# Kernel tuning notes

Hardware: AMD Instinct MI355X
Metric: run time of the kernel (lower is better)

The kernel has to match this reference:

```python
import jax, jax.numpy as jnp
import numpy as np
import math

B, S, D, H = 2, 2048, 1024, 16
HD = D // H  # 64


def setup_inputs() -> dict:
    key = jax.random.key(0)
    ks = jax.random.split(key, 12)
    s = 1.0 / math.sqrt(D)
    inp = {
        "x": jax.random.normal(ks[0], (B, S, D), dtype=jnp.float32),
        "Wq": jax.random.normal(ks[1], (D, D), dtype=jnp.float32) * s,
        "bq": jnp.zeros((D,), dtype=jnp.float32),
        "Wk": jax.random.normal(ks[2], (D, D), dtype=jnp.float32) * s,
        "bk": jnp.zeros((D,), dtype=jnp.float32),
        "Wv": jax.random.normal(ks[3], (D, D), dtype=jnp.float32) * s,
        "bv": jnp.zeros((D,), dtype=jnp.float32),
        "Wo": jax.random.normal(ks[4], (D, D), dtype=jnp.float32) * s,
        "bo": jnp.zeros((D,), dtype=jnp.float32),
        "cross_modal_weights": jnp.ones((3, 3), dtype=jnp.float32),
        "mask": jax.random.randint(ks[5], (B, S, S), 0, 2, dtype=jnp.int32),
        "modality_info": jax.random.randint(ks[6], (B, S), 0, 3, dtype=jnp.int64),
    }
    return inp


def reference(x, Wq, bq, Wk, bk, Wv, bv, Wo, bo, cross_modal_weights, mask, modality_info):
    b, s, d = x.shape
    # QKV projections -> [b, H, s, HD]
    q = (x @ Wq + bq).reshape(b, s, H, HD).transpose(0, 2, 1, 3)
    k = (x @ Wk + bk).reshape(b, s, H, HD).transpose(0, 2, 1, 3)
    v = (x @ Wv + bv).reshape(b, s, H, HD).transpose(0, 2, 1, 3)
    scores = jnp.einsum("bhqd,bhkd->bhqk", q, k) / math.sqrt(HD)
    # modality bias: torch uses .item() -> detached scalar
    modality_bias = jax.lax.stop_gradient(jnp.mean(cross_modal_weights))
    scores = scores + modality_bias
    # user mask [b, s, s] broadcast over heads; masked_fill(mask==0, -1e9)
    scores = jnp.where(mask[:, None, :, :] == 0, jnp.float32(-1e9), scores)
    attn = jax.nn.softmax(scores, axis=-1)
    # dropout_rate = 0.0 (eval) -> identity
    ctx = jnp.einsum("bhqk,bhkd->bhqd", attn, v)
    ctx = ctx.transpose(0, 2, 1, 3).reshape(b, s, d)
    return ctx @ Wo + bo
```

## Files before the change

kernel.cpp:

```cpp
#include <hip/hip_runtime.h>
#include <math.h>

#define Bdim 2
#define Sdim 2048
#define Ddim 1024
#define Hnum 16
#define HDdim 64
#define Kdim 1024

using short8   = __attribute__((ext_vector_type(8))) short;
using ushort8  = __attribute__((ext_vector_type(8))) unsigned short;
using ushort4v = __attribute__((ext_vector_type(4))) unsigned short;
using floatx4  = __attribute__((ext_vector_type(4))) float;
using half4    = __attribute__((ext_vector_type(4))) _Float16;
using half2v   = __attribute__((ext_vector_type(2))) _Float16;

__device__ __forceinline__ unsigned short f2bf(float f) {
    __bf16 b = (__bf16)f;
    return __builtin_bit_cast(unsigned short, b);
}

__device__ __forceinline__ void async_ld16(const unsigned short* g, unsigned short* l) {
    __builtin_amdgcn_global_load_lds(
        (const __attribute__((address_space(1))) unsigned int*)(g),
        (__attribute__((address_space(3))) unsigned int*)(l), 16, 0, 0);
}

__global__ __launch_bounds__(256) void prep_kernel(
    const float* __restrict__ x,
    const float* __restrict__ Wq, const float* __restrict__ Wk,
    const float* __restrict__ Wv, const float* __restrict__ Wo,
    const int* __restrict__ mask,
    unsigned short* __restrict__ xb, unsigned short* __restrict__ Wt,
    unsigned long long* __restrict__ packed)
{
    __shared__ float tile[64][65];
    const int bid = blockIdx.x;
    const int t   = threadIdx.x;

    if (bid < 2048) {
        size_t i = ((size_t)bid * 256 + t) * 8;
        float4 a = *(const float4*)(x + i);
        float4 b = *(const float4*)(x + i + 4);
        ushort8 o;
        o[0] = f2bf(a.x); o[1] = f2bf(a.y); o[2] = f2bf(a.z); o[3] = f2bf(a.w);
        o[4] = f2bf(b.x); o[5] = f2bf(b.y); o[6] = f2bf(b.z); o[7] = f2bf(b.w);
        *(ushort8*)(xb + i) = o;
    } else if (bid < 3072) {
        const int idx = bid - 2048;
        const int n0 = (idx & 15) * 64;
        const int k0 = ((idx >> 4) & 15) * 64;
        const int z  = idx >> 8;
        const float* W = (z == 0) ? Wq : (z == 1) ? Wk : (z == 2) ? Wv : Wo;
        unsigned short* outp = Wt + (size_t)z * Kdim * Ddim;
#pragma unroll
        for (int i = 0; i < 4; ++i) {
            int flat = i * 256 + t;
            int r = flat >> 4;
            int c = (flat & 15) * 4;
            float4 v = *(const float4*)(W + (size_t)(k0 + r) * Ddim + n0 + c);
            tile[r][c] = v.x; tile[r][c+1] = v.y; tile[r][c+2] = v.z; tile[r][c+3] = v.w;
        }
        __syncthreads();
#pragma unroll
        for (int i = 0; i < 16; ++i) {
            int flat = i * 256 + t;
            int n = flat >> 6;
            int k = flat & 63;
            outp[(size_t)(n0 + n) * Kdim + k0 + k] = f2bf(tile[k][n]);
        }
    } else {
        const int lane = t & 63;
        const int l15  = lane & 15;
        const int quad = lane >> 4;
        const unsigned int gid = (bid - 3072) * 4 + (t >> 6);
        const int b  = gid >> 14;
        const int qg = (gid >> 7) & 127;
        const int kb = gid & 127;
        int4 mv = *(const int4*)(mask + ((size_t)(b * Sdim) + qg * 16 + l15) * Sdim + kb * 16 + quad * 4);
        unsigned long long w0 = __ballot(mv.x != 0);
        unsigned long long w1 = __ballot(mv.y != 0);
        unsigned long long w2 = __ballot(mv.z != 0);
        unsigned long long w3 = __ballot(mv.w != 0);
        if (lane == 0) {
            unsigned long long* dst = packed + (size_t)gid * 4;
            dst[0] = w0; dst[1] = w1; dst[2] = w2; dst[3] = w3;
        }
    }
}

#define MFMA_NORM(MT, NT) acc[MT][NT] = __builtin_amdgcn_mfma_f32_16x16x32_bf16(af[MT], bfr[NT], acc[MT][NT], 0, 0, 0)
#define MFMA_SWAP(MT, NT) acc[MT][NT] = __builtin_amdgcn_mfma_f32_16x16x32_bf16(bfr[NT], af[MT], acc[MT][NT], 0, 0, 0)

#define GEMM_KLOOP(APTR, WPTR, NT_TILES, MFMA_STMT)                              \
    for (int kt = 0; kt < 16; ++kt) {                                            \
        const int k0 = kt * 64;                                                  \
        __syncthreads();                                                         \
        _Pragma("unroll")                                                        \
        for (int i = 0; i < 4; ++i) {                                            \
            int flat = i * 256 + t;                                              \
            int row  = flat >> 3;                                                \
            int cg   = (flat & 7) ^ (row & 7);                                   \
            async_ld16(APTR + (size_t)(m0 + row) * Kdim + k0 + cg * 8,           \
                       As + flat * 8);                                           \
        }                                                                        \
        _Pragma("unroll")                                                        \
        for (int i = 0; i < NT_TILES; ++i) {                                     \
            int flat = i * 256 + t;                                              \
            int row  = flat >> 3;                                                \
            int cg   = (flat & 7) ^ (row & 7);                                   \
            async_ld16(WPTR + (size_t)row * Kdim + k0 + cg * 8,                  \
                       Bs + flat * 8);                                           \
        }                                                                        \
        __syncthreads();                                                         \
        _Pragma("unroll")                                                        \
        for (int ks = 0; ks < 2; ++ks) {                                         \
            short8 af[4], bfr[NT_TILES];                                         \
            _Pragma("unroll")                                                    \
            for (int mt = 0; mt < 4; ++mt) {                                     \
                int row = wm * 64 + mt * 16 + l15;                               \
                int ch  = (ks * 4 + quad) ^ (row & 7);                           \
                af[mt] = *(const short8*)(As + row * 64 + ch * 8);               \
            }                                                                    \
            _Pragma("unroll")                                                    \
            for (int nt = 0; nt < NT_TILES; ++nt) {                              \
                int row = wn * (NT_TILES * 16) + nt * 16 + l15;                  \
                int ch  = (ks * 4 + quad) ^ (row & 7);                           \
                bfr[nt] = *(const short8*)(Bs + row * 64 + ch * 8);              \
            }                                                                    \
            _Pragma("unroll")                                                    \
            for (int mt = 0; mt < 4; ++mt)                                       \
                _Pragma("unroll")                                                \
                for (int nt = 0; nt < NT_TILES; ++nt)                            \
                    MFMA_STMT(mt, nt);                                           \
        }                                                                        \
    }

__global__ __launch_bounds__(256, 4) void qkv_mfma_kernel(
    const unsigned short* __restrict__ A, const unsigned short* __restrict__ Wt,
    const float* __restrict__ bq, const float* __restrict__ bk, const float* __restrict__ bv,
    unsigned short* __restrict__ qo, unsigned short* __restrict__ ko, _Float16* __restrict__ vto)
{
    __shared__ __align__(16) unsigned short As[128 * 64];
    __shared__ __align__(16) unsigned short Bs[128 * 64];
    const int lin = blockIdx.y * 24 + blockIdx.x;
    const int xcd = lin & 7;
    const int idx = lin >> 3;
    const int bx  = (xcd & 1) * 12 + idx % 12;
    const int by  = (xcd >> 1) * 8 + idx / 12;
    const int n0   = bx * 128;
    const int m0   = by * 128;
    const int wsel = n0 >> 10;
    const int c0   = n0 & 1023;
    const unsigned short* Wp = Wt + (size_t)wsel * Kdim * Ddim + (size_t)c0 * Kdim;

    const int t    = threadIdx.x;
    const int lane = t & 63;
    const int w    = t >> 6;
    const int quad = lane >> 4;
    const int l15  = lane & 15;
    const int wm   = w & 1;
    const int wn   = w >> 1;
    floatx4 acc[4][4];
#pragma unroll
    for (int mt = 0; mt < 4; ++mt)
#pragma unroll
        for (int nt = 0; nt < 4; ++nt) acc[mt][nt] = (floatx4){0.f, 0.f, 0.f, 0.f};

    if (wsel < 2) {
        GEMM_KLOOP(A, Wp, 4, MFMA_SWAP)
        const float* bias = wsel ? bk : bq;
        unsigned short* outp = wsel ? ko : qo;
        const float qsc = wsel ? 1.0f : 0.18033688011112042f;
#pragma unroll
        for (int mt = 0; mt < 4; ++mt) {
            int m    = m0 + wm * 64 + mt * 16 + l15;
            int bidx = m >> 11;
            int s    = m & 2047;
#pragma unroll
            for (int nt = 0; nt < 4; ++nt) {
                int c = c0 + wn * 64 + nt * 16 + quad * 4;
                float4 bb = *(const float4*)(bias + c);
                int h  = c >> 6;
                int hd = c & 63;
                ushort4v o;
                o[0] = f2bf((acc[mt][nt][0] + bb.x) * qsc);
                o[1] = f2bf((acc[mt][nt][1] + bb.y) * qsc);
                o[2] = f2bf((acc[mt][nt][2] + bb.z) * qsc);
                o[3] = f2bf((acc[mt][nt][3] + bb.w) * qsc);
                *(ushort4v*)(outp + ((size_t)(bidx * Hnum + h) * Sdim + s) * HDdim + hd) = o;
            }
        }
    } else {
        GEMM_KLOOP(A, Wp, 4, MFMA_NORM)
#pragma unroll
        for (int nt = 0; nt < 4; ++nt) {
            int c = c0 + wn * 64 + nt * 16 + l15;
            float bb = bv[c];
            int h  = c >> 6;
            int hd = c & 63;
#pragma unroll
            for (int mt = 0; mt < 4; ++mt) {
                int m    = m0 + wm * 64 + mt * 16 + quad * 4;
                int bidx = m >> 11;
                int s    = m & 2047;
                half4 o;
#pragma unroll
                for (int r = 0; r < 4; ++r) o[r] = (_Float16)(acc[mt][nt][r] + bb);
                *(half4*)(vto + ((size_t)(bidx * Hnum + h) * HDdim + hd) * Sdim + s) = o;
            }
        }
    }
}

__global__ __launch_bounds__(256, 4) void out_mfma_kernel(
    const unsigned short* __restrict__ A, const unsigned short* __restrict__ Wt,
    const float* __restrict__ bias, float* __restrict__ out)
{
    __shared__ __align__(16) unsigned short As[128 * 64];
    __shared__ __align__(16) unsigned short Bs[64 * 64];
    const int lin = blockIdx.y * 16 + blockIdx.x;
    const int xcd = lin & 7;
    const int idx = lin >> 3;
    const int bx  = idx & 15;
    const int by  = xcd * 4 + (idx >> 4);
    const int n0 = bx * 64;
    const int m0 = by * 128;
    const unsigned short* Wp = Wt + (size_t)3 * Kdim * Ddim + (size_t)n0 * Kdim;

    const int t    = threadIdx.x;
    const int lane = t & 63;
    const int w    = t >> 6;
    const int quad = lane >> 4;
    const int l15  = lane & 15;
    const int wm   = w & 1;
    const int wn   = w >> 1;
    floatx4 acc[4][2];
#pragma unroll
    for (int mt = 0; mt < 4; ++mt)
#pragma unroll
        for (int nt = 0; nt < 2; ++nt) acc[mt][nt] = (floatx4){0.f, 0.f, 0.f, 0.f};

    GEMM_KLOOP(A, Wp, 2, MFMA_SWAP)

#pragma unroll
    for (int mt = 0; mt < 4; ++mt) {
        int m = m0 + wm * 64 + mt * 16 + l15;
#pragma unroll
        for (int nt = 0; nt < 2; ++nt) {
            int c = n0 + wn * 32 + nt * 16 + quad * 4;
            float4 bb = *(const float4*)(bias + c);
            float4 o = make_float4(acc[mt][nt][0] + bb.x, acc[mt][nt][1] + bb.y,
                                   acc[mt][nt][2] + bb.z, acc[mt][nt][3] + bb.w);
            *(float4*)(out + (size_t)m * Ddim + c) = o;
        }
    }
}

__global__ __launch_bounds__(256, 4) void attn_mfma_kernel(
    const unsigned short* __restrict__ q, const unsigned short* __restrict__ k,
    const _Float16* __restrict__ vt, const unsigned long long* __restrict__ pmask,
    unsigned short* __restrict__ ctx)
{
    __shared__ __align__(16) unsigned short Ks[2][64 * 64];
    __shared__ __align__(16) _Float16       Vs[2][64 * 64];

    const int t    = threadIdx.x;
    const int w    = t >> 6;
    const int lane = t & 63;
    const int quad = lane >> 4;
    const int l15  = lane & 15;
    const int bid  = blockIdx.x;
    const int bh   = bid & 31;
    const int qseg = bid >> 5;
    const int b    = bh >> 4;
    const int h    = bh & 15;
    const int wq   = w & 1;
    const int wk   = w >> 1;
    const int qrow0 = qseg * 64 + wq * 32;

    const unsigned short* qp = q  + (size_t)bh * Sdim * HDdim;
    const unsigned short* kp = k  + (size_t)bh * Sdim * HDdim;
    const _Float16*       vp = vt + (size_t)bh * HDdim * Sdim;

    const int qg0 = __builtin_amdgcn_readfirstlane(qrow0 >> 4);
    const int wku = __builtin_amdgcn_readfirstlane(wk);
    const unsigned long long* __restrict__ pm =
        pmask + ((size_t)(b * 128 + qg0) * 128) * 4 + wku * 8;

    short8 qf[2][2];
#pragma unroll
    for (int g = 0; g < 2; ++g)
#pragma unroll
        for (int ks = 0; ks < 2; ++ks)
            qf[g][ks] = *(const short8*)(qp + (size_t)(qrow0 + g * 16 + l15) * HDdim + ks * 32 + quad * 8);

    floatx4 acc[2][4];
    floatx4 accl[2];
#pragma unroll
    for (int g = 0; g < 2; ++g) {
        accl[g] = (floatx4){0.f, 0.f, 0.f, 0.f};
#pragma unroll
        for (int hs = 0; hs < 4; ++hs) acc[g][hs] = (floatx4){0.f, 0.f, 0.f, 0.f};
    }
    const half4 ones = {(_Float16)1.f, (_Float16)1.f, (_Float16)1.f, (_Float16)1.f};

    auto stage = [&](int buf, int key0) {
#pragma unroll
        for (int i = 0; i < 2; ++i) {
            int flat = i * 256 + t;
            int row  = flat >> 3;
            int cg   = (flat & 7) ^ (row & 7);
            async_ld16(kp + (size_t)(key0 + row) * HDdim + cg * 8, &Ks[buf][flat * 8]);
        }
#pragma unroll
        for (int i = 0; i < 2; ++i) {
            int flat = i * 256 + t;
            int row  = flat >> 3;
            int cg   = (flat & 7) ^ (row & 7);
            async_ld16((const unsigned short*)(vp + (size_t)row * Sdim + key0 + cg * 8),
                       (unsigned short*)&Vs[buf][flat * 8]);
        }
    };

    stage(0, 0);

#pragma unroll 2
    for (int kt = 0; kt < 32; ++kt) {
        const int cur = kt & 1;
        __syncthreads();
        if (kt < 31) stage(cur ^ 1, (kt + 1) * 64);

        short8 kf[2][2];
#pragma unroll
        for (int ks = 0; ks < 2; ++ks)
#pragma unroll
            for (int sub = 0; sub < 2; ++sub) {
                int row = wk * 32 + sub * 16 + l15;
                int ch  = (ks * 4 + quad) ^ (row & 7);
                kf[ks][sub] = *(const short8*)&Ks[cur][row * 64 + ch * 8];
            }
        half4 vf[4][2];
#pragma unroll
        for (int hs = 0; hs < 4; ++hs)
#pragma unroll
            for (int c = 0; c < 2; ++c) {
                int row = hs * 16 + l15;
                int cc  = (wk * 2 + c) * 2 + (quad >> 1);
                int ch  = cc ^ (row & 7);
                vf[hs][c] = *(const half4*)&Vs[cur][row * 64 + ch * 8 + (quad & 1) * 4];
            }

        floatx4 sc[2][2];
#pragma unroll
        for (int g = 0; g < 2; ++g)
#pragma unroll
            for (int sub = 0; sub < 2; ++sub) sc[g][sub] = (floatx4){0.f, 0.f, 0.f, 0.f};
        __builtin_amdgcn_s_setprio(1);
#pragma unroll
        for (int ks = 0; ks < 2; ++ks)
#pragma unroll
            for (int sub = 0; sub < 2; ++sub)
#pragma unroll
                for (int g = 0; g < 2; ++g)
                    sc[g][sub] = __builtin_amdgcn_mfma_f32_16x16x32_bf16(
                        kf[ks][sub], qf[g][ks], sc[g][sub], 0, 0, 0);
        __builtin_amdgcn_s_setprio(0);

        half4 pf[2][2];
#pragma unroll
        for (int g = 0; g < 2; ++g) {
            const unsigned long long* __restrict__ pg = pm + g * 512 + kt * 16;
#pragma unroll
            for (int c = 0; c < 2; ++c) {
                float pv[4];
#pragma unroll
                for (int r = 0; r < 4; ++r) {
                    float p = exp2f(sc[g][c][r]);
                    unsigned long long wmask = pg[c * 4 + r];
                    asm("v_cndmask_b32 %0, 0, %1, %2" : "=v"(pv[r]) : "v"(p), "s"(wmask));
                }
                half2v lo = __builtin_bit_cast(half2v, __builtin_amdgcn_cvt_pkrtz(pv[0], pv[1]));
                half2v hi = __builtin_bit_cast(half2v, __builtin_amdgcn_cvt_pkrtz(pv[2], pv[3]));
                pf[g][c][0] = lo[0]; pf[g][c][1] = lo[1];
                pf[g][c][2] = hi[0]; pf[g][c][3] = hi[1];
            }
        }

        __builtin_amdgcn_s_setprio(1);
#pragma unroll
        for (int c = 0; c < 2; ++c) {
#pragma unroll
            for (int hs = 0; hs < 4; ++hs)
#pragma unroll
                for (int g = 0; g < 2; ++g)
                    acc[g][hs] = __builtin_amdgcn_mfma_f32_16x16x16f16(
                        vf[hs][c], pf[g][c], acc[g][hs], 0, 0, 0);
#pragma unroll
            for (int g = 0; g < 2; ++g)
                accl[g] = __builtin_amdgcn_mfma_f32_16x16x16f16(
                    ones, pf[g][c], accl[g], 0, 0, 0);
        }
        __builtin_amdgcn_s_setprio(0);
    }

    __syncthreads();
    float* red  = (float*)&Ks[0][0];
    float* redl = (float*)&Vs[0][0];
    if (wk == 1) {
#pragma unroll
        for (int g = 0; g < 2; ++g) {
#pragma unroll
            for (int hs = 0; hs < 4; ++hs)
                *(floatx4*)&red[((((wq * 2) + g) * 4 + hs) * 64 + lane) * 4] = acc[g][hs];
            redl[(wq * 2 + g) * 64 + lane] = accl[g][0];
        }
    }
    __syncthreads();
    if (wk == 0) {
#pragma unroll
        for (int g = 0; g < 2; ++g) {
            float lsum = accl[g][0] + redl[(wq * 2 + g) * 64 + lane];
            float inv  = 1.0f / fmaxf(lsum, 1e-30f);
            int row = qrow0 + g * 16 + l15;
#pragma unroll
            for (int hs = 0; hs < 4; ++hs) {
                floatx4 o4 = acc[g][hs] + *(const floatx4*)&red[((((wq * 2) + g) * 4 + hs) * 64 + lane) * 4];
                ushort4v o;
#pragma unroll
                for (int r = 0; r < 4; ++r) o[r] = f2bf(o4[r] * inv);
                *(ushort4v*)(ctx + (size_t)(b * Sdim + row) * Ddim + h * 64 + hs * 16 + quad * 4) = o;
            }
        }
    }
}

extern "C" void kernel_launch(void* const* d_in, const int* in_sizes, int n_in,
                              void* d_out, int out_size, void* d_ws, size_t ws_size,
                              hipStream_t stream) {
    const float* x   = (const float*)d_in[0];
    const float* Wq  = (const float*)d_in[1];
    const float* bq  = (const float*)d_in[2];
    const float* Wk  = (const float*)d_in[3];
    const float* bk  = (const float*)d_in[4];
    const float* Wv  = (const float*)d_in[5];
    const float* bv  = (const float*)d_in[6];
    const float* Wo  = (const float*)d_in[7];
    const float* bo  = (const float*)d_in[8];
    const int*  mask = (const int*)d_in[10];
    float* out = (float*)d_out;

    char* ws = (char*)d_ws;
    unsigned short* xb  = (unsigned short*)(ws);
    unsigned short* Wt  = (unsigned short*)(ws + (size_t)8  * 1048576);
    unsigned short* qb  = (unsigned short*)(ws + (size_t)16 * 1048576);
    unsigned short* kb  = (unsigned short*)(ws + (size_t)24 * 1048576);
    _Float16*       vtb = (_Float16*)     (ws + (size_t)32 * 1048576);
    unsigned long long* pmk = (unsigned long long*)(ws + (size_t)40 * 1048576);
    unsigned short* ctxb = xb;

    prep_kernel<<<dim3(11264), 256, 0, stream>>>(x, Wq, Wk, Wv, Wo, mask, xb, Wt, pmk);
    qkv_mfma_kernel<<<dim3(24, 32), 256, 0, stream>>>(xb, Wt, bq, bk, bv, qb, kb, vtb);
    attn_mfma_kernel<<<dim3(1024), 256, 0, stream>>>(qb, kb, vtb, pmk, ctxb);
    out_mfma_kernel<<<dim3(16, 32), 256, 0, stream>>>(ctxb, Wt, bo, out);
}
```

Baseline: 232.1 us.

## Widen attention blocks to 512 threads sharing each K/V tile across 128 queries

The attention kernel now runs 8 waves per block: 4 query groups by 2 key halves. Each block covers 128 query rows instead of 64, so every staged K/V tile in LDS is reused by twice as many queries, and global-to-LDS traffic and the grid size are both halved. Each thread now issues one async load each for K and V. The cross-wave reduction is split across both LDS buffers, and a separate array holds the row sums. Launch bounds of (512, 4) may force a lower per-thread register budget and cause spills, and the grid now has fewer, larger blocks.

```diff
diff --git a/kernel.cpp b/kernel.cpp
--- a/kernel.cpp
+++ b/kernel.cpp
@@ -257,13 +257,14 @@
     }
 }
 
-__global__ __launch_bounds__(256, 4) void attn_mfma_kernel(
+__global__ __launch_bounds__(512, 4) void attn_mfma_kernel(
     const unsigned short* __restrict__ q, const unsigned short* __restrict__ k,
     const _Float16* __restrict__ vt, const unsigned long long* __restrict__ pmask,
     unsigned short* __restrict__ ctx)
 {
     __shared__ __align__(16) unsigned short Ks[2][64 * 64];
     __shared__ __align__(16) _Float16       Vs[2][64 * 64];
+    __shared__ float redl[512];
 
     const int t    = threadIdx.x;
     const int w    = t >> 6;
@@ -275,9 +276,9 @@
     const int qseg = bid >> 5;
     const int b    = bh >> 4;
     const int h    = bh & 15;
-    const int wq   = w & 1;
-    const int wk   = w >> 1;
-    const int qrow0 = qseg * 64 + wq * 32;
+    const int wq   = w & 3;
+    const int wk   = w >> 2;
+    const int qrow0 = qseg * 128 + wq * 32;
 
     const unsigned short* qp = q  + (size_t)bh * Sdim * HDdim;
     const unsigned short* kp = k  + (size_t)bh * Sdim * HDdim;
@@ -306,21 +307,11 @@
     const half4 ones = {(_Float16)1.f, (_Float16)1.f, (_Float16)1.f, (_Float16)1.f};
 
     auto stage = [&](int buf, int key0) {
-#pragma unroll
-        for (int i = 0; i < 2; ++i) {
-            int flat = i * 256 + t;
-            int row  = flat >> 3;
-            int cg   = (flat & 7) ^ (row & 7);
-            async_ld16(kp + (size_t)(key0 + row) * HDdim + cg * 8, &Ks[buf][flat * 8]);
-        }
-#pragma unroll
-        for (int i = 0; i < 2; ++i) {
-            int flat = i * 256 + t;
-            int row  = flat >> 3;
-            int cg   = (flat & 7) ^ (row & 7);
-            async_ld16((const unsigned short*)(vp + (size_t)row * Sdim + key0 + cg * 8),
-                       (unsigned short*)&Vs[buf][flat * 8]);
-        }
+        int row = t >> 3;
+        int cg  = (t & 7) ^ (row & 7);
+        async_ld16(kp + (size_t)(key0 + row) * HDdim + cg * 8, &Ks[buf][t * 8]);
+        async_ld16((const unsigned short*)(vp + (size_t)row * Sdim + key0 + cg * 8),
+                   (unsigned short*)&Vs[buf][t * 8]);
     };
 
     stage(0, 0);
@@ -405,14 +396,17 @@
     }
 
     __syncthreads();
-    float* red  = (float*)&Ks[0][0];
-    float* redl = (float*)&Vs[0][0];
+    float* redA = (float*)&Ks[0][0];
+    float* redB = (float*)&Vs[0][0];
     if (wk == 1) {
 #pragma unroll
         for (int g = 0; g < 2; ++g) {
 #pragma unroll
-            for (int hs = 0; hs < 4; ++hs)
-                *(floatx4*)&red[((((wq * 2) + g) * 4 + hs) * 64 + lane) * 4] = acc[g][hs];
+            for (int hs = 0; hs < 4; ++hs) {
+                float* dst = (hs < 2) ? redA : redB;
+                int slot = ((wq * 2 + g) * 2 + (hs & 1)) * 64 + lane;
+                *(floatx4*)&dst[slot * 4] = acc[g][hs];
+            }
             redl[(wq * 2 + g) * 64 + lane] = accl[g][0];
         }
     }
@@ -425,7 +419,9 @@
             int row = qrow0 + g * 16 + l15;
 #pragma unroll
             for (int hs = 0; hs < 4; ++hs) {
-                floatx4 o4 = acc[g][hs] + *(const floatx4*)&red[((((wq * 2) + g) * 4 + hs) * 64 + lane) * 4];
+                const float* src = (hs < 2) ? redA : redB;
+                int slot = ((wq * 2 + g) * 2 + (hs & 1)) * 64 + lane;
+                floatx4 o4 = acc[g][hs] + *(const floatx4*)&src[slot * 4];
                 ushort4v o;
 #pragma unroll
                 for (int r = 0; r < 4; ++r) o[r] = f2bf(o4[r] * inv);
@@ -461,6 +457,6 @@
 
     prep_kernel<<<dim3(11264), 256, 0, stream>>>(x, Wq, Wk, Wv, Wo, mask, xb, Wt, pmk);
     qkv_mfma_kernel<<<dim3(24, 32), 256, 0, stream>>>(xb, Wt, bq, bk, bv, qb, kb, vtb);
-    attn_mfma_kernel<<<dim3(1024), 256, 0, stream>>>(qb, kb, vtb, pmk, ctxb);
+    attn_mfma_kernel<<<dim3(512), 512, 0, stream>>>(qb, kb, vtb, pmk, ctxb);
     out_mfma_kernel<<<dim3(16, 32), 256, 0, stream>>>(ctxb, Wt, bo, out);
 }
```

Result: no change. 229.4 us (median of 2 runs) (-1.2%).
